# Kernel optimization log

Measured on AMD Instinct MI355X. Metric: run time of the kernel, lower is better.

## Reference

```python
import jax, jax.numpy as jnp
import numpy as np

EMBED_DIM = 1024
BATCH = 4
SEQ = 2048


def setup_inputs() -> dict:
    key = jax.random.key(0)
    ks = jax.random.split(key, 9)
    D = EMBED_DIM
    s = 1.0 / np.sqrt(D)
    inputs = jax.random.normal(ks[0], (BATCH, SEQ, D), dtype=jnp.float32)
    rotation_params = jax.random.normal(ks[1], (D, D), dtype=jnp.float32) * s
    entangle_params = jax.random.normal(ks[2], (D, D), dtype=jnp.float32) * s
    Wq = jax.random.normal(ks[3], (D, D), dtype=jnp.float32) * s
    bq = jax.random.normal(ks[4], (D,), dtype=jnp.float32) * 0.01
    Wk = jax.random.normal(ks[5], (D, D), dtype=jnp.float32) * s
    bk = jax.random.normal(ks[6], (D,), dtype=jnp.float32) * 0.01
    Wv = jax.random.normal(ks[7], (D, D), dtype=jnp.float32) * s
    bv = jax.random.normal(ks[8], (D,), dtype=jnp.float32) * 0.01
    # causal mask: True = masked out (matches torch masked_fill semantics)
    mask = jnp.triu(jnp.ones((SEQ, SEQ), dtype=bool), k=1)
    return {"inputs": inputs, "rotation_params": rotation_params,
            "entangle_params": entangle_params, "Wq": Wq, "bq": bq,
            "Wk": Wk, "bk": bk, "Wv": Wv, "bv": bv, "mask": mask}


def reference(inputs, rotation_params, entangle_params, Wq, bq, Wk, bk, Wv, bv, mask):
    D = inputs.shape[-1]
    # q = Linear(x) @ R^T ; k = Linear(x) @ E^T ; v = Linear(x)
    q = (jnp.einsum('bsd,ed->bse', inputs, Wq) + bq) @ rotation_params.T
    k = (jnp.einsum('bsd,ed->bse', inputs, Wk) + bk) @ entangle_params.T
    v = jnp.einsum('bsd,ed->bse', inputs, Wv) + bv
    scores = jnp.einsum('bqd,bkd->bqk', q, k) / jnp.sqrt(jnp.float32(D))
    scores = jnp.where(mask, jnp.float32(-jnp.inf), scores)
    probs = jax.nn.softmax(scores, axis=-1)  # dropout=0.0 -> identity
    return jnp.einsum('bqk,bkd->bqd', probs, v)
```

## Files before the change

### kernel.cpp

```cpp
#include <hip/hip_runtime.h>
#include <hip/hip_bf16.h>
#include <stdint.h>

#define DD 1024
#define SS 2048
#define BB 4

typedef __bf16 bf16;
typedef __bf16 bf16x8 __attribute__((ext_vector_type(8)));
typedef __bf16 bf16x4 __attribute__((ext_vector_type(4)));
typedef float f32x4 __attribute__((ext_vector_type(4)));

__device__ __forceinline__ void gload_lds16(const bf16* g, bf16* l) {
  __builtin_amdgcn_global_load_lds(
      (const __attribute__((address_space(1))) void*)g,
      (__attribute__((address_space(3))) void*)l, 16, 0, 0);
}

__global__ __launch_bounds__(256) void prep_all(
    const float* __restrict__ x, const float* __restrict__ R,
    const float* __restrict__ E, const float* __restrict__ Wv,
    const float* __restrict__ Wq, const float* __restrict__ Wk,
    const float* __restrict__ bq, const float* __restrict__ bk,
    const float* __restrict__ bv, bf16* __restrict__ xb,
    bf16* __restrict__ Rb, bf16* __restrict__ Eb, bf16* __restrict__ Wvb,
    bf16* __restrict__ WqT, bf16* __restrict__ WkT, float* __restrict__ bias) {
  int bid = blockIdx.x;
  int t = threadIdx.x;
  if (bid < 11264) {
    const float* src;
    bf16* dst;
    int base;
    if (bid < 8192) { src = x; dst = xb; base = bid; }
    else if (bid < 9216) { src = R; dst = Rb; base = bid - 8192; }
    else if (bid < 10240) { src = E; dst = Eb; base = bid - 9216; }
    else { src = Wv; dst = Wvb; base = bid - 10240; }
    int i = (base * 256 + t) * 4;
    float4 v = *(const float4*)(src + i);
    bf16x4 o;
    o.x = (bf16)v.x; o.y = (bf16)v.y; o.z = (bf16)v.z; o.w = (bf16)v.w;
    *(bf16x4*)(dst + i) = o;
  } else if (bid < 13312) {
    int r2 = bid - 11264;
    const float* src = (r2 >= 1024) ? Wk : Wq;
    bf16* dst = (r2 >= 1024) ? WkT : WqT;
    int rem = r2 & 1023;
    int bx = rem & 31, by = rem >> 5;
    __shared__ float tile[32][33];
    int tx = t & 31, ty = t >> 5;
    int xcol = bx * 32 + tx;
    int y0 = by * 32;
    for (int r = ty; r < 32; r += 8)
      tile[r][tx] = src[(y0 + r) * DD + xcol];
    __syncthreads();
    int dx = by * 32 + tx;
    int dy0 = bx * 32;
    for (int r = ty; r < 32; r += 8)
      dst[(dy0 + r) * DD + dx] = (bf16)tile[tx][r];
  } else {
    int e = bid - 13312;
    if (e >= 2048) { if (t == 0) bias[e] = bv[e - 2048]; return; }
    const float* M = (e < 1024) ? R : E;
    const float* bb = (e < 1024) ? bq : bk;
    int row = e & 1023;
    float s = 0.f;
    for (int f = t; f < DD; f += 256) s += M[row * DD + f] * bb[f];
    for (int o = 32; o >= 1; o >>= 1) s += __shfl_xor(s, o, 64);
    __shared__ float red[4];
    if ((t & 63) == 0) red[t >> 6] = s;
    __syncthreads();
    if (t == 0) bias[e] = red[0] + red[1] + red[2] + red[3];
  }
}

template <int MODE>
__global__ __launch_bounds__(256, 4)
void gemm_bt(const bf16* __restrict__ Ag, long lda, long sAb,
             const bf16* __restrict__ Bg, long ldb, long sBb,
             void* __restrict__ Cg, long ldc, long sCb,
             const float* __restrict__ bias, float scale, int K,
             bf16* __restrict__ vTp) {
  __shared__ __align__(16) bf16 smem[16384];
  bf16* As = smem;
  bf16* Bs = smem + 8192;

  int bx = blockIdx.x, by = blockIdx.y, bz = blockIdx.z;
  if (MODE == 1 && bx > by) return;
  long m0 = (long)by * 128, n0 = (long)bx * 128;
  const bf16* A = Ag + (long)bz * sAb + m0 * lda;
  const bf16* Bp = Bg + (long)bz * sBb + n0 * ldb;

  int t = threadIdx.x;
  int w = t >> 6, l = t & 63;
  int lr = l >> 2;
  int lc = (((l & 3) ^ (lr & 3)) * 8);
  int quad = l >> 4, ln = l & 15;
  int wm = w >> 1, wn = w & 1;
  int rdoff = ((quad ^ (ln & 3)) * 8);

  int Keff = (MODE == 2) ? (by + 1) * 128 : K;

  f32x4 acc[4][4];
#pragma unroll
  for (int i = 0; i < 4; i++)
#pragma unroll
    for (int j = 0; j < 4; j++) acc[i][j] = f32x4{0.f, 0.f, 0.f, 0.f};

  const bf16* a_base = As + (wm * 64 + ln) * 32 + rdoff;
  const bf16* b_base = Bs + (wn * 64 + ln) * 32 + rdoff;
  long arow0 = (long)(w * 16 + lr);

  for (int k0 = 0; k0 < Keff; k0 += 64) {
#pragma unroll
    for (int kk = 0; kk < 2; kk++) {
      int kc = k0 + kk * 32 + lc;
      gload_lds16(A + arow0 * lda + kc, As + kk * 4096 + w * 512);
      gload_lds16(A + (arow0 + 64) * lda + kc, As + kk * 4096 + 2048 + w * 512);
      gload_lds16(Bp + arow0 * ldb + kc, Bs + kk * 4096 + w * 512);
      gload_lds16(Bp + (arow0 + 64) * ldb + kc, Bs + kk * 4096 + 2048 + w * 512);
    }
    asm volatile("s_waitcnt vmcnt(0)" ::: "memory");
    __syncthreads();

#pragma unroll
    for (int kk = 0; kk < 2; kk++) {
      bf16x8 af[4], bfr[4];
#pragma unroll
      for (int i = 0; i < 4; i++) {
        af[i] = *(const bf16x8*)(a_base + kk * 4096 + i * 512);
        bfr[i] = *(const bf16x8*)(b_base + kk * 4096 + i * 512);
      }
#pragma unroll
      for (int i = 0; i < 4; i++)
#pragma unroll
        for (int j = 0; j < 4; j++)
          acc[i][j] = __builtin_amdgcn_mfma_f32_16x16x32_bf16(
              af[i], bfr[j], acc[i][j], 0, 0, 0);
    }
    __syncthreads();
  }

  if (MODE == 0) {
    if (vTp && n0 >= 2048) {
      int d0 = (int)n0 - 2048;
      int b = (int)(m0 >> 11);
      int s0 = (int)(m0 & 2047);
#pragma unroll
      for (int i = 0; i < 4; i++) {
        int sb = wm * 64 + i * 16 + quad * 4;
#pragma unroll
        for (int j = 0; j < 4; j++) {
          int d = wn * 64 + j * 16 + ln;
          float bv_ = bias[n0 + d];
#pragma unroll
          for (int r = 0; r < 4; r++)
            smem[d * 128 + ((sb + r) ^ (ln << 3))] = (bf16)(acc[i][j][r] + bv_);
        }
      }
      __syncthreads();
      int d = t >> 1, h = t & 1;
      bf16* dst = vTp + (long)b * DD * SS + (long)(d0 + d) * SS + s0 + h * 64;
#pragma unroll
      for (int j = 0; j < 8; j++) {
        int sbase = h * 64 + j * 8;
        bf16x8 v = *(const bf16x8*)(smem + d * 128 + (sbase ^ ((d & 15) << 3)));
        *(bf16x8*)(dst + j * 8) = v;
      }
    } else {
      bf16* C = (bf16*)Cg + (long)bz * sCb + m0 * ldc + n0;
#pragma unroll
      for (int i = 0; i < 4; i++) {
        int rb = wm * 64 + i * 16 + quad * 4;
#pragma unroll
        for (int j = 0; j < 4; j++) {
          int col = wn * 64 + j * 16 + ln;
          float bv_ = bias ? bias[n0 + col] : 0.f;
#pragma unroll
          for (int r = 0; r < 4; r++)
            C[(long)(rb + r) * ldc + col] = (bf16)(acc[i][j][r] + bv_);
        }
      }
    }
  } else {
    float* C = (float*)Cg + (long)bz * sCb + m0 * ldc + n0;
#pragma unroll
    for (int i = 0; i < 4; i++) {
      int rb = wm * 64 + i * 16 + quad * 4;
#pragma unroll
      for (int j = 0; j < 4; j++) {
        int col = wn * 64 + j * 16 + ln;
#pragma unroll
        for (int r = 0; r < 4; r++) {
          int row = rb + r;
          if (MODE == 1) {
            if (n0 + col <= m0 + row)
              C[(long)row * ldc + col] = acc[i][j][r] * scale;
          } else {
            C[(long)row * ldc + col] = acc[i][j][r];
          }
        }
      }
    }
  }
}

__global__ __launch_bounds__(256) void softmax_rows(float* __restrict__ scores) {
  long m = (long)blockIdx.x * 4 + (threadIdx.x >> 6);
  int l = threadIdx.x & 63;
  int nvalid = (int)(m & (SS - 1)) + 1;
  float* row = scores + m * SS;

  float xv[32];
#pragma unroll
  for (int c = 0; c < 8; c++) {
    int base = c * 256 + l * 4;
    float4 v = {0.f, 0.f, 0.f, 0.f};
    if (base < nvalid) v = *(const float4*)(row + base);
    xv[c * 4 + 0] = v.x; xv[c * 4 + 1] = v.y;
    xv[c * 4 + 2] = v.z; xv[c * 4 + 3] = v.w;
  }

  float mx = -INFINITY;
#pragma unroll
  for (int c = 0; c < 8; c++) {
    int base = c * 256 + l * 4;
#pragma unroll
    for (int j = 0; j < 4; j++)
      if (base + j < nvalid) mx = fmaxf(mx, xv[c * 4 + j]);
  }
  for (int o = 32; o >= 1; o >>= 1) mx = fmaxf(mx, __shfl_xor(mx, o, 64));

  float e[32];
  float sum = 0.f;
#pragma unroll
  for (int c = 0; c < 8; c++) {
    int base = c * 256 + l * 4;
#pragma unroll
    for (int j = 0; j < 4; j++) {
      float ev = (base + j < nvalid) ? __expf(xv[c * 4 + j] - mx) : 0.f;
      e[c * 4 + j] = ev;
      sum += ev;
    }
  }
  for (int o = 32; o >= 1; o >>= 1) sum += __shfl_xor(sum, o, 64);
  float inv = 1.f / sum;

  bf16* brow = (bf16*)row;
#pragma unroll
  for (int c = 0; c < 8; c++) {
    int base = c * 256 + l * 4;
    bf16x4 o4;
#pragma unroll
    for (int j = 0; j < 4; j++) o4[j] = (bf16)(e[c * 4 + j] * inv);
    *(bf16x4*)(brow + base) = o4;
  }
}

extern "C" void kernel_launch(void* const* d_in, const int* in_sizes, int n_in,
                              void* d_out, int out_size, void* d_ws,
                              size_t ws_size, hipStream_t stream) {
  const float* x = (const float*)d_in[0];
  const float* R = (const float*)d_in[1];
  const float* E = (const float*)d_in[2];
  const float* Wq = (const float*)d_in[3];
  const float* bq = (const float*)d_in[4];
  const float* Wk = (const float*)d_in[5];
  const float* bk = (const float*)d_in[6];
  const float* Wv = (const float*)d_in[7];
  const float* bv = (const float*)d_in[8];
  float* out = (float*)d_out;

  char* ws = (char*)d_ws;
  bf16* qkv = (bf16*)ws;
  bf16* vT = (bf16*)(ws + 50331648);
  float* scores = (float*)(ws + 67108864);
  char* sr = ws + 67108864;
  bf16* xb = (bf16*)sr;
  bf16* Rb = (bf16*)(sr + 16777216);
  bf16* WqT = (bf16*)(sr + 20971520);
  bf16* wcat = (bf16*)(sr + 25165824);
  float* bias = (float*)(sr + 31457280);
  bf16* Eb = Rb + 1024 * 1024;
  bf16* WkT = WqT + 1024 * 1024;

  prep_all<<<16384, 256, 0, stream>>>(x, R, E, Wv, Wq, Wk, bq, bk, bv, xb, Rb,
                                      Eb, wcat + 2048 * DD, WqT, WkT, bias);

  gemm_bt<0><<<dim3(8, 8, 2), 256, 0, stream>>>(
      Rb, DD, 1024 * 1024, WqT, DD, 1024 * 1024, wcat, DD, 1024 * 1024,
      nullptr, 1.f, DD, nullptr);

  gemm_bt<0><<<dim3(24, 64, 1), 256, 0, stream>>>(xb, DD, 0, wcat, DD, 0, qkv,
                                                  3072, 0, bias, 1.f, DD, vT);

  gemm_bt<1><<<dim3(16, 16, BB), 256, 0, stream>>>(
      qkv, 3072, (long)SS * 3072, qkv + 1024, 3072, (long)SS * 3072, scores,
      SS, (long)SS * SS, nullptr, 0.03125f, DD, nullptr);

  softmax_rows<<<BB * SS / 4, 256, 0, stream>>>(scores);

  gemm_bt<2><<<dim3(8, 16, BB), 256, 0, stream>>>(
      (const bf16*)scores, 4096, (long)SS * 4096, vT, SS, (long)DD * SS, out,
      DD, (long)SS * DD, nullptr, 1.f, SS, nullptr);
}
```

Measured before the change: 308.8 us.

## Fuse softmax exp into QK^T GEMM epilogue and defer normalization to PV GEMM

```diff
diff --git a/kernel.cpp b/kernel.cpp
--- a/kernel.cpp
+++ b/kernel.cpp
@@ -1,6 +1,7 @@
 #include <hip/hip_runtime.h>
 #include <hip/hip_bf16.h>
 #include <stdint.h>
+#include <math.h>
 
 #define DD 1024
 #define SS 2048
@@ -24,7 +25,8 @@
     const float* __restrict__ bq, const float* __restrict__ bk,
     const float* __restrict__ bv, bf16* __restrict__ xb,
     bf16* __restrict__ Rb, bf16* __restrict__ Eb, bf16* __restrict__ Wvb,
-    bf16* __restrict__ WqT, bf16* __restrict__ WkT, float* __restrict__ bias) {
+    bf16* __restrict__ WqT, bf16* __restrict__ WkT, float* __restrict__ bias,
+    float* __restrict__ rowsums) {
   int bid = blockIdx.x;
   int t = threadIdx.x;
   if (bid < 11264) {
@@ -57,7 +59,7 @@
     int dy0 = bx * 32;
     for (int r = ty; r < 32; r += 8)
       dst[(dy0 + r) * DD + dx] = (bf16)tile[tx][r];
-  } else {
+  } else if (bid < 16384) {
     int e = bid - 13312;
     if (e >= 2048) { if (t == 0) bias[e] = bv[e - 2048]; return; }
     const float* M = (e < 1024) ? R : E;
@@ -70,6 +72,9 @@
     if ((t & 63) == 0) red[t >> 6] = s;
     __syncthreads();
     if (t == 0) bias[e] = red[0] + red[1] + red[2] + red[3];
+  } else {
+    int idx = (bid - 16384) * 256 + t;
+    rowsums[idx] = 0.f;
   }
 }
 
@@ -79,13 +84,20 @@
              const bf16* __restrict__ Bg, long ldb, long sBb,
              void* __restrict__ Cg, long ldc, long sCb,
              const float* __restrict__ bias, float scale, int K,
-             bf16* __restrict__ vTp) {
+             bf16* __restrict__ vTp, float* __restrict__ rowsums) {
   __shared__ __align__(16) bf16 smem[16384];
   bf16* As = smem;
   bf16* Bs = smem + 8192;
 
   int bx = blockIdx.x, by = blockIdx.y, bz = blockIdx.z;
-  if (MODE == 1 && bx > by) return;
+  if (MODE == 1) {
+    int q = bx;
+    by = (int)((sqrtf(8.f * q + 1.f) - 1.f) * 0.5f);
+    while ((by + 1) * (by + 2) / 2 <= q) by++;
+    while (by * (by + 1) / 2 > q) by--;
+    bx = q - by * (by + 1) / 2;
+  }
+  if (MODE == 2) by = 15 - by;
   long m0 = (long)by * 128, n0 = (long)bx * 128;
   const bf16* A = Ag + (long)bz * sAb + m0 * lda;
   const bf16* Bp = Bg + (long)bz * sBb + n0 * ldb;
@@ -181,78 +193,53 @@
         }
       }
     }
+  } else if (MODE == 1) {
+#pragma unroll
+    for (int i = 0; i < 4; i++) {
+      int rb = wm * 64 + i * 16 + quad * 4;
+#pragma unroll
+      for (int j = 0; j < 4; j++) {
+        int col = wn * 64 + j * 16 + ln;
+#pragma unroll
+        for (int r = 0; r < 4; r++) {
+          int row = rb + r;
+          float p = 0.f;
+          if (n0 + col <= m0 + row) p = __expf(acc[i][j][r] * scale);
+          smem[row * 128 + (col ^ ((row & 15) << 3))] = (bf16)p;
+        }
+      }
+    }
+    __syncthreads();
+    int row = t >> 1, h = t & 1;
+    bf16* P = (bf16*)Cg + (long)bz * sCb + (m0 + row) * ldc + n0;
+    float rsum = 0.f;
+#pragma unroll
+    for (int jj = 0; jj < 8; jj++) {
+      int p8 = h * 8 + jj;
+      int slot = p8 ^ (row & 15);
+      bf16x8 v = *(const bf16x8*)(smem + row * 128 + slot * 8);
+#pragma unroll
+      for (int e = 0; e < 8; e++) rsum += (float)v[e];
+      *(bf16x8*)(P + p8 * 8) = v;
+    }
+    atomicAdd(&rowsums[(long)bz * SS + m0 + row], rsum);
   } else {
     float* C = (float*)Cg + (long)bz * sCb + m0 * ldc + n0;
+    const float* rs = rowsums + (long)bz * SS + m0;
 #pragma unroll
     for (int i = 0; i < 4; i++) {
       int rb = wm * 64 + i * 16 + quad * 4;
+      float inv[4];
+#pragma unroll
+      for (int r = 0; r < 4; r++) inv[r] = 1.f / rs[rb + r];
 #pragma unroll
       for (int j = 0; j < 4; j++) {
         int col = wn * 64 + j * 16 + ln;
 #pragma unroll
-        for (int r = 0; r < 4; r++) {
-          int row = rb + r;
-          if (MODE == 1) {
-            if (n0 + col <= m0 + row)
-              C[(long)row * ldc + col] = acc[i][j][r] * scale;
-          } else {
-            C[(long)row * ldc + col] = acc[i][j][r];
-          }
-        }
-      }
-    }
-  }
-}
-
-__global__ __launch_bounds__(256) void softmax_rows(float* __restrict__ scores) {
-  long m = (long)blockIdx.x * 4 + (threadIdx.x >> 6);
-  int l = threadIdx.x & 63;
-  int nvalid = (int)(m & (SS - 1)) + 1;
-  float* row = scores + m * SS;
-
-  float xv[32];
-#pragma unroll
-  for (int c = 0; c < 8; c++) {
-    int base = c * 256 + l * 4;
-    float4 v = {0.f, 0.f, 0.f, 0.f};
-    if (base < nvalid) v = *(const float4*)(row + base);
-    xv[c * 4 + 0] = v.x; xv[c * 4 + 1] = v.y;
-    xv[c * 4 + 2] = v.z; xv[c * 4 + 3] = v.w;
-  }
-
-  float mx = -INFINITY;
-#pragma unroll
-  for (int c = 0; c < 8; c++) {
-    int base = c * 256 + l * 4;
-#pragma unroll
-    for (int j = 0; j < 4; j++)
-      if (base + j < nvalid) mx = fmaxf(mx, xv[c * 4 + j]);
-  }
-  for (int o = 32; o >= 1; o >>= 1) mx = fmaxf(mx, __shfl_xor(mx, o, 64));
-
-  float e[32];
-  float sum = 0.f;
-#pragma unroll
-  for (int c = 0; c < 8; c++) {
-    int base = c * 256 + l * 4;
-#pragma unroll
-    for (int j = 0; j < 4; j++) {
-      float ev = (base + j < nvalid) ? __expf(xv[c * 4 + j] - mx) : 0.f;
-      e[c * 4 + j] = ev;
-      sum += ev;
-    }
-  }
-  for (int o = 32; o >= 1; o >>= 1) sum += __shfl_xor(sum, o, 64);
-  float inv = 1.f / sum;
-
-  bf16* brow = (bf16*)row;
-#pragma unroll
-  for (int c = 0; c < 8; c++) {
-    int base = c * 256 + l * 4;
-    bf16x4 o4;
-#pragma unroll
-    for (int j = 0; j < 4; j++) o4[j] = (bf16)(e[c * 4 + j] * inv);
-    *(bf16x4*)(brow + base) = o4;
+        for (int r = 0; r < 4; r++)
+          C[(long)(rb + r) * ldc + col] = acc[i][j][r] * inv[r];
+      }
+    }
   }
 }
 
@@ -273,33 +260,34 @@
   char* ws = (char*)d_ws;
   bf16* qkv = (bf16*)ws;
   bf16* vT = (bf16*)(ws + 50331648);
-  float* scores = (float*)(ws + 67108864);
-  char* sr = ws + 67108864;
+  bf16* probs = (bf16*)(ws + 67108864);
+  float* rowsums = (float*)(ws + 100663296);
+  char* sr = ws + 101711872;
   bf16* xb = (bf16*)sr;
   bf16* Rb = (bf16*)(sr + 16777216);
+  bf16* Eb = Rb + 1024 * 1024;
   bf16* WqT = (bf16*)(sr + 20971520);
+  bf16* WkT = WqT + 1024 * 1024;
   bf16* wcat = (bf16*)(sr + 25165824);
   float* bias = (float*)(sr + 31457280);
-  bf16* Eb = Rb + 1024 * 1024;
-  bf16* WkT = WqT + 1024 * 1024;
-
-  prep_all<<<16384, 256, 0, stream>>>(x, R, E, Wv, Wq, Wk, bq, bk, bv, xb, Rb,
-                                      Eb, wcat + 2048 * DD, WqT, WkT, bias);
+
+  prep_all<<<16416, 256, 0, stream>>>(x, R, E, Wv, Wq, Wk, bq, bk, bv, xb, Rb,
+                                      Eb, wcat + 2048 * DD, WqT, WkT, bias,
+                                      rowsums);
 
   gemm_bt<0><<<dim3(8, 8, 2), 256, 0, stream>>>(
       Rb, DD, 1024 * 1024, WqT, DD, 1024 * 1024, wcat, DD, 1024 * 1024,
-      nullptr, 1.f, DD, nullptr);
+      nullptr, 1.f, DD, nullptr, nullptr);
 
   gemm_bt<0><<<dim3(24, 64, 1), 256, 0, stream>>>(xb, DD, 0, wcat, DD, 0, qkv,
-                                                  3072, 0, bias, 1.f, DD, vT);
-
-  gemm_bt<1><<<dim3(16, 16, BB), 256, 0, stream>>>(
-      qkv, 3072, (long)SS * 3072, qkv + 1024, 3072, (long)SS * 3072, scores,
-      SS, (long)SS * SS, nullptr, 0.03125f, DD, nullptr);
-
-  softmax_rows<<<BB * SS / 4, 256, 0, stream>>>(scores);
+                                                  3072, 0, bias, 1.f, DD, vT,
+                                                  nullptr);
+
+  gemm_bt<1><<<dim3(136, 1, BB), 256, 0, stream>>>(
+      qkv, 3072, (long)SS * 3072, qkv + 1024, 3072, (long)SS * 3072, probs,
+      SS, (long)SS * SS, nullptr, 0.03125f, DD, nullptr, rowsums);
 
   gemm_bt<2><<<dim3(8, 16, BB), 256, 0, stream>>>(
-      (const bf16*)scores, 4096, (long)SS * 4096, vT, SS, (long)DD * SS, out,
-      DD, (long)SS * DD, nullptr, 1.f, SS, nullptr);
-}
+      probs, SS, (long)SS * SS, vT, SS, (long)DD * SS, out,
+      DD, (long)SS * DD, nullptr, 1.f, SS, nullptr, rowsums);
+}
```

Measured after the change: 303.0 us. No clear change (-1.9%).
